# Kernel optimization log

Hardware: AMD Instinct MI355X
Metric: run time of the kernel (lower is better)

## Reference

```python
import jax, jax.numpy as jnp
import numpy as np
import math

ALPHA = 0.6
BETA = 0.4
NPTS = 1000   # trapezoid points, matches beta_cdf default npts
EPS = 1e-10   # lower integration limit, matches zeros(...) + 1e-10
# log Beta(alpha, beta) normalizer
BETALN = math.lgamma(ALPHA) + math.lgamma(BETA) - math.lgamma(ALPHA + BETA)


def beta_logpdf(x):
    # torch.distributions.Beta(ALPHA, BETA).log_prob(x)
    return (ALPHA - 1.0) * jnp.log(x) + (BETA - 1.0) * jnp.log1p(-x) - BETALN


def setup_inputs() -> dict:
    key = jax.random.key(0)
    # probabilities in (0,1); uniform like a sigmoid-gate output
    x = jax.random.uniform(key, (512, 128), dtype=jnp.float32)
    return {"x": x}


def reference(x):
    n, c = x.shape
    sorted_x = jnp.sort(x, axis=0)                                  # [n, c]
    # linspace grid from EPS to each sorted value: [NPTS, n, c]
    steps = (jnp.arange(NPTS, dtype=x.dtype) / (NPTS - 1))[:, None, None]
    grid = EPS + steps * (sorted_x - EPS)
    pdf = jnp.exp(beta_logpdf(grid))                                # [NPTS, n, c]
    # replicate torch's check: skip first point if pdf(EPS) > 1
    # (static: depends only on the fixed alpha/beta constants)
    pdf0 = math.exp((ALPHA - 1.0) * math.log(EPS)
                    + (BETA - 1.0) * math.log1p(-EPS) - BETALN)
    start = 1 if pdf0 > 1.0 else 0
    g = grid[start:]
    p = pdf[start:]
    # trapezoidal rule along the integration axis -> pcdf [n, c]
    pcdf = 0.5 * jnp.sum((p[1:] + p[:-1]) * (g[1:] - g[:-1]), axis=0)
    ecdf = (jnp.arange(1, n + 1, dtype=x.dtype) / (n + 1))[:, None]  # [n, 1]
    # sum of squared CDF gaps over all columns, divided by n
    loss = jnp.sum((pcdf - ecdf) ** 2) / n
    return loss
```

## Files before the change

### kernel.cpp

```cpp
#include <hip/hip_runtime.h>
#include <cmath>

#define N_ROWS 512
#define N_COLS 128

__device__ __forceinline__ float betacf(float a, float b, float x) {
    float qab = a + b, qap = a + 1.0f, qam = a - 1.0f;
    float c = 1.0f;
    float d = 1.0f - qab * x / qap;
    if (fabsf(d) < 1e-30f) d = 1e-30f;
    d = 1.0f / d;
    float h = d;
    #pragma unroll
    for (int m = 1; m <= 4; ++m) {
        float fm = (float)m, m2 = 2.0f * fm;
        float aa = fm * (b - fm) * x / ((qam + m2) * (a + m2));
        d = 1.0f + aa * d; if (fabsf(d) < 1e-30f) d = 1e-30f;
        c = 1.0f + aa / c; if (fabsf(c) < 1e-30f) c = 1e-30f;
        d = 1.0f / d;
        h *= d * c;
        aa = -(a + fm) * (qab + fm) * x / ((a + m2) * (qap + m2));
        d = 1.0f + aa * d; if (fabsf(d) < 1e-30f) d = 1e-30f;
        c = 1.0f + aa / c; if (fabsf(c) < 1e-30f) c = 1e-30f;
        d = 1.0f / d;
        h *= d * c;
    }
    return h;
}

__global__ __launch_bounds__(512) void sort_loss(const float* __restrict__ x,
                                                 float* __restrict__ out,
                                                 float lnB, float invB, float c_head) {
    __shared__ float sd[N_ROWS];
    const int tid = threadIdx.x;
    const int col = blockIdx.x;
    float v = x[tid * N_COLS + col];
    for (int k = 2; k <= N_ROWS; k <<= 1) {
        for (int j = k >> 1; j > 0; j >>= 1) {
            float pv;
            if (j >= 64) {
                __syncthreads();
                sd[tid] = v;
                __syncthreads();
                pv = sd[tid ^ j];
            } else {
                pv = __shfl_xor(v, j, 64);
            }
            const bool lower = (tid & j) == 0;
            const bool asc   = (tid & k) == 0;
            v = (lower == asc) ? fminf(v, pv) : fmaxf(v, pv);
        }
    }
    const float s  = fmaxf(v, 1e-30f);
    const float sm = s - 1e-10f;
    const float h  = sm * (1.0f / 999.0f);
    const float x1 = 1e-10f + h;

    const float ls  = __logf(s);
    const float om  = fmaxf(1.0f - s, 1e-30f);
    const float lom = __logf(om);
    const float bt  = __expf(fmaf(0.6f, ls, fmaf(0.4f, lom, -lnB)));

    const bool lo = s < 0.53333333f;
    const float ca = lo ? 0.6f : 0.4f;
    const float cb = lo ? 0.4f : 0.6f;
    const float cx = lo ? s : om;
    const float cf = betacf(ca, cb, cx);
    const float I  = lo ? bt * cf * (1.0f / 0.6f)
                        : 1.0f - bt * cf * (1.0f / 0.4f);

    const float head = c_head * __expf(0.6f * __logf(x1));

    const float sm04 = __expf(-0.4f * ls);
    const float f0   = __expf(-0.6f * lom);
    const float f1   = __expf(-0.6f * __logf(fmaf(1.0f, h, om)));
    const float f2   = __expf(-0.6f * __logf(fmaf(2.0f, h, om)));
    const float f3   = __expf(-0.6f * __logf(fmaf(3.0f, h, om)));
    const float w4   = fmaf(4.0f, h, om);
    const float f4   = __expf(-0.6f * __logf(w4));
    const float fsum = fmaf(0.5f, f0, f1) + f2 + fmaf(0.5f, f4, f3);
    const float w4p  = w4 * f4;
    const float w0p  = om * f0;
    const float dr   = (h * fsum - (w4p - w0p) * 2.5f) * sm04 * invB;

    const float T    = I - head + dr;
    const float ecdf = (float)(tid + 1) * (1.0f / 513.0f);
    const float d    = T - ecdf;
    float val = d * d;

    #pragma unroll
    for (int off = 32; off > 0; off >>= 1)
        val += __shfl_down(val, off);
    __syncthreads();
    if ((tid & 63) == 0) sd[tid >> 6] = val;
    __syncthreads();
    if (tid == 0) {
        float bs = 0.0f;
        #pragma unroll
        for (int w = 0; w < 8; ++w) bs += sd[w];
        atomicAdd(out, bs * (1.0f / (float)N_ROWS));
    }
}

extern "C" void kernel_launch(void* const* d_in, const int* in_sizes, int n_in,
                              void* d_out, int out_size, void* d_ws, size_t ws_size,
                              hipStream_t stream) {
    const float* x = (const float*)d_in[0];
    float* out = (float*)d_out;

    const double B = exp(lgamma(0.6) + lgamma(0.4) - lgamma(1.0));
    const float lnB    = (float)log(B);
    const float invB   = (float)(1.0 / B);
    const float c_head = (float)(1.0 / (0.6 * B) - 0.03185 / B);

    hipMemsetAsync(d_out, 0, sizeof(float), stream);
    sort_loss<<<N_COLS, N_ROWS, 0, stream>>>(x, out, lnB, invB, c_head);
}
```

Measured before the change: 61.57 us.

## Double-buffer bitonic LDS exchange and simplify continued-fraction and correction terms

The bitonic sort's cross-wavefront steps now alternate between two shared buffers, which drops one barrier per step. The incomplete-beta continued fraction uses precomputed coefficients, hardware reciprocals and no clamps. The head term reuses log(s) through a folded constant, and the trapezoid correction drops from five sample points to three. This cuts transcendental and division work, but the approximations and removed clamps may lose accuracy.

After: 61.76 us. No clear change (+0.3%).

```diff
diff --git a/kernel.cpp b/kernel.cpp
--- a/kernel.cpp
+++ b/kernel.cpp
@@ -4,45 +4,26 @@
 #define N_ROWS 512
 #define N_COLS 128
 
-__device__ __forceinline__ float betacf(float a, float b, float x) {
-    float qab = a + b, qap = a + 1.0f, qam = a - 1.0f;
-    float c = 1.0f;
-    float d = 1.0f - qab * x / qap;
-    if (fabsf(d) < 1e-30f) d = 1e-30f;
-    d = 1.0f / d;
-    float h = d;
-    #pragma unroll
-    for (int m = 1; m <= 4; ++m) {
-        float fm = (float)m, m2 = 2.0f * fm;
-        float aa = fm * (b - fm) * x / ((qam + m2) * (a + m2));
-        d = 1.0f + aa * d; if (fabsf(d) < 1e-30f) d = 1e-30f;
-        c = 1.0f + aa / c; if (fabsf(c) < 1e-30f) c = 1e-30f;
-        d = 1.0f / d;
-        h *= d * c;
-        aa = -(a + fm) * (qab + fm) * x / ((a + m2) * (qap + m2));
-        d = 1.0f + aa * d; if (fabsf(d) < 1e-30f) d = 1e-30f;
-        c = 1.0f + aa / c; if (fabsf(c) < 1e-30f) c = 1e-30f;
-        d = 1.0f / d;
-        h *= d * c;
-    }
-    return h;
-}
+__device__ __forceinline__ float rcpf(float v) { return __builtin_amdgcn_rcpf(v); }
 
 __global__ __launch_bounds__(512) void sort_loss(const float* __restrict__ x,
                                                  float* __restrict__ out,
-                                                 float lnB, float invB, float c_head) {
-    __shared__ float sd[N_ROWS];
+                                                 float lnB, float invB, float c_head2) {
+    __shared__ float sdA[N_ROWS];
+    __shared__ float sdB[N_ROWS];
     const int tid = threadIdx.x;
     const int col = blockIdx.x;
     float v = x[tid * N_COLS + col];
+
+    float* buf = sdA;
     for (int k = 2; k <= N_ROWS; k <<= 1) {
         for (int j = k >> 1; j > 0; j >>= 1) {
             float pv;
             if (j >= 64) {
+                buf[tid] = v;
                 __syncthreads();
-                sd[tid] = v;
-                __syncthreads();
-                pv = sd[tid ^ j];
+                pv = buf[tid ^ j];
+                buf = (buf == sdA) ? sdB : sdA;
             } else {
                 pv = __shfl_xor(v, j, 64);
             }
@@ -54,36 +35,51 @@
     const float s  = fmaxf(v, 1e-30f);
     const float sm = s - 1e-10f;
     const float h  = sm * (1.0f / 999.0f);
-    const float x1 = 1e-10f + h;
 
     const float ls  = __logf(s);
     const float om  = fmaxf(1.0f - s, 1e-30f);
     const float lom = __logf(om);
     const float bt  = __expf(fmaf(0.6f, ls, fmaf(0.4f, lom, -lnB)));
 
-    const bool lo = s < 0.53333333f;
-    const float ca = lo ? 0.6f : 0.4f;
-    const float cb = lo ? 0.4f : 0.6f;
+    const bool  lo = s < 0.53333333f;
     const float cx = lo ? s : om;
-    const float cf = betacf(ca, cb, cx);
-    const float I  = lo ? bt * cf * (1.0f / 0.6f)
-                        : 1.0f - bt * cf * (1.0f / 0.4f);
+    const float r0 = lo ? 0.625f       : 0.71428573f;
+    const float e1 = lo ? -0.14423077f : -0.11904762f;
+    const float o1 = lo ? -0.34188035f : -0.34313726f;
+    const float e2 = lo ? -0.19323671f : -0.18716577f;
+    const float o2 = lo ? -0.30279503f : -0.30303031f;
+    const float e3 = lo ? -0.21103896f : -0.20833333f;
+    const float o3 = lo ? -0.28708133f : -0.28716215f;
+    const float e4 = lo ? -0.22031824f : -0.21879020f;
+    const float o4 = lo ? -0.27858528f : -0.27862209f;
 
-    const float head = c_head * __expf(0.6f * __logf(x1));
+    float rd  = rcpf(fmaf(-r0, cx, 1.0f));
+    float hcf = rd;
+    float cr  = 1.0f;
+    #define CF_HALF(COEF) { \
+        const float aa = (COEF) * cx; \
+        const float dn = fmaf(aa, rd, 1.0f); rd = rcpf(dn); \
+        const float cn = fmaf(aa, cr, 1.0f); cr = rcpf(cn); \
+        hcf *= rd * cn; }
+    CF_HALF(e1) CF_HALF(o1) CF_HALF(e2) CF_HALF(o2)
+    CF_HALF(e3) CF_HALF(o3) CF_HALF(e4) CF_HALF(o4)
+    #undef CF_HALF
+
+    const float I = lo ? bt * hcf * 1.6666667f
+                       : 1.0f - bt * hcf * 2.5f;
+
+    const float head = c_head2 * __expf(0.6f * ls);
 
     const float sm04 = __expf(-0.4f * ls);
     const float f0   = __expf(-0.6f * lom);
-    const float f1   = __expf(-0.6f * __logf(fmaf(1.0f, h, om)));
-    const float f2   = __expf(-0.6f * __logf(fmaf(2.0f, h, om)));
-    const float f3   = __expf(-0.6f * __logf(fmaf(3.0f, h, om)));
-    const float w4   = fmaf(4.0f, h, om);
-    const float f4   = __expf(-0.6f * __logf(w4));
-    const float fsum = fmaf(0.5f, f0, f1) + f2 + fmaf(0.5f, f4, f3);
-    const float w4p  = w4 * f4;
-    const float w0p  = om * f0;
-    const float dr   = (h * fsum - (w4p - w0p) * 2.5f) * sm04 * invB;
+    const float w1   = om + h;
+    const float f1   = __expf(-0.6f * __logf(w1));
+    const float w2   = fmaf(2.0f, h, om);
+    const float f2   = __expf(-0.6f * __logf(w2));
+    const float fsum = fmaf(0.5f, f0 + f2, f1);
+    const float drc  = (h * fsum - (w2 * f2 - om * f0) * 2.5f) * sm04 * invB;
 
-    const float T    = I - head + dr;
+    const float T    = I - head + drc;
     const float ecdf = (float)(tid + 1) * (1.0f / 513.0f);
     const float d    = T - ecdf;
     float val = d * d;
@@ -91,13 +87,12 @@
     #pragma unroll
     for (int off = 32; off > 0; off >>= 1)
         val += __shfl_down(val, off);
-    __syncthreads();
-    if ((tid & 63) == 0) sd[tid >> 6] = val;
+    if ((tid & 63) == 0) sdA[tid >> 6] = val;
     __syncthreads();
     if (tid == 0) {
         float bs = 0.0f;
         #pragma unroll
-        for (int w = 0; w < 8; ++w) bs += sd[w];
+        for (int w = 0; w < 8; ++w) bs += sdA[w];
         atomicAdd(out, bs * (1.0f / (float)N_ROWS));
     }
 }
@@ -111,8 +106,8 @@
     const double B = exp(lgamma(0.6) + lgamma(0.4) - lgamma(1.0));
     const float lnB    = (float)log(B);
     const float invB   = (float)(1.0 / B);
-    const float c_head = (float)(1.0 / (0.6 * B) - 0.03185 / B);
+    const float c_head2 = (float)((1.0 / (0.6 * B) - 0.03185 / B) * pow(999.0, -0.6));
 
     hipMemsetAsync(d_out, 0, sizeof(float), stream);
-    sort_loss<<<N_COLS, N_ROWS, 0, stream>>>(x, out, lnB, invB, c_head);
+    sort_loss<<<N_COLS, N_ROWS, 0, stream>>>(x, out, lnB, invB, c_head2);
 }
```
